# Kernel optimization log

Measured on AMD Instinct MI355X. Metric: run time of the kernel, lower is better.

## Reference

```python
import jax, jax.numpy as jnp
import numpy as np

B, F, T, H, LBL, NT = 64, 128, 1024, 256, 4, 11
S = T * LBL  # CRF sequence length


def setup_inputs() -> dict:
    key = jax.random.key(0)
    ks = iter(jax.random.split(key, 40))
    rn = lambda shape, s=1.0: jax.random.normal(next(ks), shape, jnp.float32) * s
    x = rn((B, F, T))
    lengths = jax.random.randint(next(ks), (B,), 1, T + 1)
    lengths = lengths.at[0].set(T)  # max(batch_length) == T
    labels = jax.random.randint(next(ks), (B, S), 0, NT)
    valid = jnp.arange(S)[None, :] < (lengths * LBL)[:, None]
    y_true = jnp.where(valid, labels, -1)
    sc = 0.05
    return dict(
        x=x, y_true=y_true, lengths=lengths,
        h0=rn((4, B, H)), c0=rn((4, B, H)),
        w_ih_l0=rn((4 * H, F), sc), w_hh_l0=rn((4 * H, H), sc), b_l0=rn((4 * H,), sc),
        w_ih_l0r=rn((4 * H, F), sc), w_hh_l0r=rn((4 * H, H), sc), b_l0r=rn((4 * H,), sc),
        w_ih_l1=rn((4 * H, 2 * H), sc), w_hh_l1=rn((4 * H, H), sc), b_l1=rn((4 * H,), sc),
        w_ih_l1r=rn((4 * H, 2 * H), sc), w_hh_l1r=rn((4 * H, H), sc), b_l1r=rn((4 * H,), sc),
        w_out=rn((LBL * NT, 2 * H), sc), b_out=rn((LBL * NT,), sc),
        start_trans=rn((NT,), 0.1), end_trans=rn((NT,), 0.1), trans=rn((NT, NT), 0.1),
    )


def _lstm_dir(x, h0, c0, w_ih, w_hh, b):
    # x: [B,T,Din] -> hs: [B,T,H]; PyTorch gate order i,f,g,o
    xg = jnp.einsum('btd,gd->btg', x, w_ih) + b  # [B,T,4H]

    def step(carry, xt):
        h, c = carry
        g = xt + h @ w_hh.T
        i, f, gg, o = jnp.split(g, 4, axis=-1)
        c = jax.nn.sigmoid(f) * c + jax.nn.sigmoid(i) * jnp.tanh(gg)
        h = jax.nn.sigmoid(o) * jnp.tanh(c)
        return (h, c), h

    _, hs = jax.lax.scan(step, (h0, c0), jnp.swapaxes(xg, 0, 1))
    return jnp.swapaxes(hs, 0, 1)


def _bilayer(x, rev_idx, h0f, c0f, h0b, c0b, pf, pb):
    hf = _lstm_dir(x, h0f, c0f, *pf)
    xr = jnp.take_along_axis(x, rev_idx[:, :, None], axis=1)  # per-sample reverse within length
    hbr = _lstm_dir(xr, h0b, c0b, *pb)
    hb = jnp.take_along_axis(hbr, rev_idx[:, :, None], axis=1)
    return jnp.concatenate([hf, hb], axis=-1)


def _crf_llh(em, tags, mask, start, end, trans):
    # em [B,S,NT], tags [B,S] (-1 pad), mask [B,S] bool. torchcrf sum-reduction llh.
    tc = jnp.where(mask, tags, 0)
    bidx = jnp.arange(em.shape[0])
    first = start[tc[:, 0]] + em[bidx, 0, tc[:, 0]]
    em_sc = jnp.take_along_axis(em, tc[:, :, None], axis=2)[..., 0]  # [B,S]
    tr_sc = trans[tc[:, :-1], tc[:, 1:]]  # [B,S-1]
    num = first + jnp.sum((tr_sc + em_sc[:, 1:]) * mask[:, 1:], axis=1)
    seq_ends = jnp.sum(mask, axis=1) - 1
    num = num + end[tc[bidx, seq_ends]]

    def step(alpha, inp):
        e, m = inp  # e [B,NT], m [B]
        nxt = jax.nn.logsumexp(alpha[:, :, None] + trans[None] + e[:, None, :], axis=1)
        return jnp.where(m[:, None], nxt, alpha), None

    alpha0 = start[None] + em[:, 0]
    alpha, _ = jax.lax.scan(step, alpha0, (jnp.swapaxes(em[:, 1:], 0, 1), mask[:, 1:].T))
    logZ = jax.nn.logsumexp(alpha + end[None], axis=1)
    return jnp.sum(num - logZ)


def _viterbi(em, mask, start, end, trans):
    def step(score, inp):
        e, m = inp
        nxt = score[:, :, None] + trans[None] + e[:, None, :]  # [B,NT,NT]
        best, idx = jnp.max(nxt, axis=1), jnp.argmax(nxt, axis=1)
        return jnp.where(m[:, None], best, score), idx

    score0 = start[None] + em[:, 0]
    final, hist = jax.lax.scan(step, score0, (jnp.swapaxes(em[:, 1:], 0, 1), mask[:, 1:].T))
    last = jnp.argmax(final + end[None], axis=1)  # [B]

    def back(carry, inp):
        h, m = inp  # h [B,NT], m [B]
        prev = jnp.take_along_axis(h, carry[:, None], axis=1)[:, 0]
        carry = jnp.where(m, prev, carry)
        return carry, carry

    _, ys = jax.lax.scan(back, last, (hist, mask[:, 1:].T), reverse=True)  # [S-1,B]
    return jnp.concatenate([ys.T, last[:, None]], axis=1)  # [B,S]


def reference(x, y_true, lengths, h0, c0,
              w_ih_l0, w_hh_l0, b_l0, w_ih_l0r, w_hh_l0r, b_l0r,
              w_ih_l1, w_hh_l1, b_l1, w_ih_l1r, w_hh_l1r, b_l1r,
              w_out, b_out, start_trans, end_trans, trans):
    xt = jnp.transpose(x, (0, 2, 1))  # [B,T,F]
    t = jnp.arange(T)
    rev_idx = jnp.where(t[None, :] < lengths[:, None], lengths[:, None] - 1 - t[None, :], t[None, :])
    l0 = _bilayer(xt, rev_idx, h0[0], c0[0], h0[1], c0[1],
                  (w_ih_l0, w_hh_l0, b_l0), (w_ih_l0r, w_hh_l0r, b_l0r))
    l1 = _bilayer(l0, rev_idx, h0[2], c0[2], h0[3], c0[3],
                  (w_ih_l1, w_hh_l1, b_l1), (w_ih_l1r, w_hh_l1r, b_l1r))
    feats = l1 * (t[None, :] < lengths[:, None])[:, :, None].astype(l1.dtype)  # pad -> 0 like pad_packed_sequence
    em = (feats @ w_out.T + b_out).reshape(B, S, NT)
    mask = y_true != -1
    loss = -_crf_llh(em, y_true, mask, start_trans, end_trans, trans) / B
    decoded = _viterbi(em, mask, start_trans, end_trans, trans)
    return loss, decoded
```

## Files before the change

### kernel.cpp

```cpp
#include <hip/hip_runtime.h>
#include <hip/hip_bf16.h>

typedef _Float16 f16x8 __attribute__((ext_vector_type(8)));
typedef float f32x4 __attribute__((ext_vector_type(4)));

#define DI static __device__ __forceinline__

constexpr int Bn = 64, Fn = 128, Tn = 1024, Hn = 256, NTn = 11;
constexpr int BT = Bn * Tn;
constexpr int Gn = 4 * Hn;
constexpr int Sn = 4 * Tn;

__device__ __align__(16) _Float16 g_xt_h[BT * Fn];
__device__ __align__(16) _Float16 g_xt_l[BT * Fn];
__device__ __align__(16) _Float16 g_f0_h[BT * 512];
__device__ __align__(16) _Float16 g_f0_l[BT * 512];
__device__ __align__(16) _Float16 g_f1_h[BT * 512];
__device__ __align__(16) _Float16 g_f1_l[BT * 512];
__device__ __align__(16) float    g_xg[(size_t)BT * 2048];
__device__ __align__(16) _Float16 g_whh_h[4 * Gn * Hn];
__device__ __align__(16) _Float16 g_whh_l[4 * Gn * Hn];
__device__ __align__(16) _Float16 g_wih0_h[2048 * Fn];
__device__ __align__(16) _Float16 g_wih0_l[2048 * Fn];
__device__ __align__(16) _Float16 g_wih1_h[2048 * 512];
__device__ __align__(16) _Float16 g_wih1_l[2048 * 512];
__device__ __align__(16) _Float16 g_wout_h[48 * 512];
__device__ __align__(16) _Float16 g_wout_l[48 * 512];
__device__ float g_b0[2048], g_b1[2048], g_bo[48];
__device__ float g_em[BT * 44];
__device__ __align__(4) unsigned char g_hist[(size_t)Sn * Bn * NTn];
__device__ int   g_rev[BT];
__device__ float g_llh[Bn];
__device__ int   g_last[Bn];
__device__ unsigned int g_hxs[2][4][2][4096];
__device__ int g_syncp[2][4][2][8][2][16];

DI f32x4 mfma_(f16x8 a, f16x8 b, f32x4 c) {
  return __builtin_amdgcn_mfma_f32_16x16x32_f16(a, b, c, 0, 0, 0);
}
DI float sigf(float x) { return 1.f / (1.f + __expf(-x)); }
DI float tanh_(float x) { return 1.f - 2.f / (1.f + __expf(2.f * x)); }

__global__ void k_zinit() {
  int i = blockIdx.x * 256 + threadIdx.x;
  if (i < 2 * 4 * 2 * 8 * 2 * 16) ((int*)g_syncp)[i] = 0;
}

__global__ void k_split(const float* __restrict__ src, int which, int off, int n) {
  int i = blockIdx.x * 256 + threadIdx.x;
  if (i >= n) return;
  float v = src[i];
  _Float16 h = (_Float16)v;
  _Float16 l = (_Float16)(v - (float)h);
  _Float16 *H, *L;
  switch (which) {
    case 1:  H = g_wih0_h; L = g_wih0_l; break;
    case 2:  H = g_wih1_h; L = g_wih1_l; break;
    default: H = g_wout_h; L = g_wout_l; break;
  }
  H[off + i] = h; L[off + i] = l;
}

__global__ void k_wswz(const float* __restrict__ w0, const float* __restrict__ w1,
                       const float* __restrict__ w2, const float* __restrict__ w3) {
  int i = blockIdx.x * 256 + threadIdx.x;
  if (i >= 4 * Gn * Hn) return;
  int mat = i >> 18;
  int e = i & 262143;
  int nt = e >> 12, rem = e & 4095;
  int kc = rem >> 9;
  int rem2 = rem & 511;
  int lane = rem2 >> 3, j = rem2 & 7;
  int row = nt * 16 + (lane & 15);
  int col = kc * 32 + (lane >> 4) * 8 + j;
  const float* src = mat == 0 ? w0 : mat == 1 ? w1 : mat == 2 ? w2 : w3;
  float v = src[row * Hn + col];
  _Float16 h = (_Float16)v;
  g_whh_h[i] = h;
  g_whh_l[i] = (_Float16)(v - (float)h);
}

__global__ void k_copy(const float* __restrict__ src, int which, int off, int n) {
  int i = blockIdx.x * 256 + threadIdx.x;
  if (i >= n) return;
  float* D = which == 0 ? g_b0 : which == 1 ? g_b1 : g_bo;
  D[off + i] = src[i];
}

__global__ void k_pad() {
  int i = blockIdx.x * 256 + threadIdx.x;
  if (i < 48 * 512 - 44 * 512) {
    g_wout_h[44 * 512 + i] = (_Float16)0.f;
    g_wout_l[44 * 512 + i] = (_Float16)0.f;
  }
  if (i < 4) g_bo[44 + i] = 0.f;
}

__global__ void k_rev(const int* __restrict__ lengths) {
  int i = blockIdx.x * 256 + threadIdx.x;
  if (i >= BT) return;
  int b = i >> 10, t = i & 1023;
  int len = lengths[b];
  int r = (t < len) ? (len - 1 - t) : t;
  g_rev[i] = (b << 10) | r;
}

__global__ void k_xpose(const float* __restrict__ x) {
  __shared__ float tile[32][33];
  int t0 = blockIdx.x * 32, d0 = blockIdx.y * 32, b = blockIdx.z;
  int tx = threadIdx.x, ty = threadIdx.y;
  #pragma unroll
  for (int i = 0; i < 4; i++) {
    int d = d0 + ty + i * 8;
    tile[ty + i * 8][tx] = x[((size_t)b * Fn + d) * Tn + t0 + tx];
  }
  __syncthreads();
  #pragma unroll
  for (int i = 0; i < 4; i++) {
    int t = t0 + ty + i * 8;
    float v = tile[tx][ty + i * 8];
    _Float16 h = (_Float16)v;
    size_t o = ((size_t)b * Tn + t) * Fn + d0 + tx;
    g_xt_h[o] = h;
    g_xt_l[o] = (_Float16)(v - (float)h);
  }
}

template <int SEL, int NPL>
__global__ __launch_bounds__(256) void k_gemm() {
  constexpr int KD = SEL == 0 ? 128 : 512;
  constexpr int WM = SEL == 2 ? 4 : 2;
  constexpr int WN = SEL == 2 ? 1 : 2;
  constexpr int MW = SEL == 2 ? 2 : 4;
  constexpr int NW = SEL == 2 ? 3 : 4;
  constexpr int LDO = SEL == 2 ? 44 : 2048;
  constexpr int NCOL = SEL == 2 ? 44 : 2048;
  constexpr int NSPLIT = SEL == 2 ? (1 << 30) : 1024;
  const _Float16* Ah = SEL == 0 ? g_xt_h : SEL == 1 ? g_f0_h : g_f1_h;
  const _Float16* Al = SEL == 0 ? g_xt_l : SEL == 1 ? g_f0_l : g_f1_l;
  const _Float16* Bh = SEL == 0 ? g_wih0_h : SEL == 1 ? g_wih1_h : g_wout_h;
  const _Float16* Bl = SEL == 0 ? g_wih0_l : SEL == 1 ? g_wih1_l : g_wout_l;
  const float* bias = SEL == 0 ? g_b0 : SEL == 1 ? g_b1 : g_bo;
  float* out = SEL == 2 ? g_em : g_xg;

  const int lane = threadIdx.x & 63, wv = threadIdx.x >> 6;
  const int wm = wv / WN, wn = wv % WN;
  const int c = lane & 15, q = lane >> 4;
  const int bm0 = blockIdx.x * (WM * MW * 16);
  const int bn0 = blockIdx.y * (WN * NW * 16);
  const bool bw = bn0 >= NSPLIT;
  int arow[MW];
  #pragma unroll
  for (int mi = 0; mi < MW; mi++) {
    int r = bm0 + (wm * MW + mi) * 16 + c;
    arow[mi] = bw ? g_rev[r] : r;
  }
  f32x4 acc[MW][NW];
  #pragma unroll
  for (int mi = 0; mi < MW; mi++)
    #pragma unroll
    for (int ni = 0; ni < NW; ni++) acc[mi][ni] = f32x4{0.f, 0.f, 0.f, 0.f};

  for (int kc = 0; kc < KD / 32; kc++) {
    const int k = kc * 32 + q * 8;
    f16x8 ah[MW], al[MW], bh[NW], bl[NW];
    #pragma unroll
    for (int mi = 0; mi < MW; mi++) {
      ah[mi] = *(const f16x8*)(Ah + (size_t)arow[mi] * KD + k);
      if constexpr (NPL > 1) al[mi] = *(const f16x8*)(Al + (size_t)arow[mi] * KD + k);
    }
    #pragma unroll
    for (int ni = 0; ni < NW; ni++) {
      int n = bn0 + (wn * NW + ni) * 16 + c;
      bh[ni] = *(const f16x8*)(Bh + (size_t)n * KD + k);
      if constexpr (NPL > 1) bl[ni] = *(const f16x8*)(Bl + (size_t)n * KD + k);
    }
    #pragma unroll
    for (int mi = 0; mi < MW; mi++)
      #pragma unroll
      for (int ni = 0; ni < NW; ni++) {
        acc[mi][ni] = mfma_(ah[mi], bh[ni], acc[mi][ni]);
        if constexpr (NPL > 1) {
          acc[mi][ni] = mfma_(ah[mi], bl[ni], acc[mi][ni]);
          acc[mi][ni] = mfma_(al[mi], bh[ni], acc[mi][ni]);
        }
      }
  }
  #pragma unroll
  for (int mi = 0; mi < MW; mi++)
    #pragma unroll
    for (int ni = 0; ni < NW; ni++) {
      int col = bn0 + (wn * NW + ni) * 16 + c;
      if (col < NCOL) {
        int row0 = bm0 + (wm * MW + mi) * 16 + q * 4;
        float bv = bias[col];
        #pragma unroll
        for (int r = 0; r < 4; r++)
          out[(size_t)(row0 + r) * LDO + col] = acc[mi][ni][r] + bv;
      }
    }
}

__global__ __launch_bounds__(512, 1) void k_rec3(const float* __restrict__ h0,
                                                 const float* __restrict__ c0, int layer) {
  __shared__ __align__(16) _Float16 Wh_l[8][8][512];
  __shared__ __align__(16) _Float16 Wl_l[8][8][512];
  __shared__ __align__(16) _Float16 lh[4096], ll[4096];
  __shared__ float gbuf[2][3][16][16];
  const int tid = threadIdx.x, lane = tid & 63, w = tid >> 6;
  const int c = lane & 15, q = lane >> 4;
  const int bg = blockIdx.x, d = blockIdx.y, s = blockIdx.z;
  const int dirIdx = layer * 2 + d;
  const int g = w >> 1, hm = w & 1;
  const int m = 2 * s + hm;
  const int nt = g * 16 + m;
  const int u = m * 16 + c;
  const _Float16* whp = g_whh_h + (size_t)dirIdx * (Gn * Hn);
  const _Float16* wlp = g_whh_l + (size_t)dirIdx * (Gn * Hn);
  _Float16* fh = layer ? g_f1_h : g_f0_h;
  _Float16* fl = layer ? g_f1_l : g_f0_l;
  const float* h0p = h0 + ((size_t)dirIdx * Bn + bg * 16) * Hn;
  const float* c0p = c0 + ((size_t)dirIdx * Bn + bg * 16) * Hn;

  #pragma unroll
  for (int kc = 0; kc < 8; kc++) {
    *(f16x8*)&Wh_l[w][kc][lane * 8] =
        *(const f16x8*)(whp + ((size_t)(nt * 8 + kc) * 64 + lane) * 8);
    *(f16x8*)&Wl_l[w][kc][lane * 8] =
        *(const f16x8*)(wlp + ((size_t)(nt * 8 + kc) * 64 + lane) * 8);
  }
  for (int i = tid; i < 4096; i += 512) {
    int j = i & 7, ln = (i >> 3) & 63, kc = i >> 9;
    int row = ln & 15, uu = kc * 32 + ((ln >> 4) * 8) + j;
    float v = h0p[row * Hn + uu];
    _Float16 hv = (_Float16)v;
    lh[i] = hv;
    ll[i] = (_Float16)(v - (float)hv);
  }
  float creg[4];
  if (g == 0) {
    #pragma unroll
    for (int r = 0; r < 4; r++) creg[r] = c0p[(4 * q + r) * Hn + u];
  }
  size_t xoff[4];
  #pragma unroll
  for (int r = 0; r < 4; r++)
    xoff[r] = ((size_t)(bg * 16 + 4 * q + r) * Tn) * 2048 + (size_t)d * 1024;
  const int col = g * 256 + u;
  const int fb = (((u >> 5) * 64 + ((u >> 3) & 3) * 16) * 8) + (u & 7);

  float xgv[4];
  #pragma unroll
  for (int r = 0; r < 4; r++) xgv[r] = g_xg[xoff[r] + col];
  __syncthreads();

  for (int t = 0; t < Tn; t++) {
    f32x4 acc;
    #pragma unroll
    for (int r = 0; r < 4; r++) acc[r] = xgv[r];

    #pragma unroll
    for (int kc = 0; kc < 8; kc++) {
      f16x8 ah = *(const f16x8*)(lh + (kc * 64 + lane) * 8);
      f16x8 al = *(const f16x8*)(ll + (kc * 64 + lane) * 8);
      f16x8 wh = *(const f16x8*)&Wh_l[w][kc][lane * 8];
      f16x8 wl = *(const f16x8*)&Wl_l[w][kc][lane * 8];
      acc = mfma_(ah, wh, acc);
      acc = mfma_(ah, wl, acc);
      acc = mfma_(al, wh, acc);
    }

    if (g != 0) {
      #pragma unroll
      for (int r = 0; r < 4; r++) gbuf[hm][g - 1][4 * q + r][c] = acc[r];
    }
    __syncthreads();

    const bool more = (t + 1 < Tn);
    if (g == 0) {
      _Float16 hvs[4], lvs[4];
      #pragma unroll
      for (int r = 0; r < 4; r++) {
        float gi = acc[r];
        float gf = gbuf[hm][0][4 * q + r][c];
        float gg = gbuf[hm][1][4 * q + r][c];
        float go = gbuf[hm][2][4 * q + r][c];
        float cn = sigf(gf) * creg[r] + sigf(gi) * tanh_(gg);
        float hn = sigf(go) * tanh_(cn);
        creg[r] = cn;
        hvs[r] = (_Float16)hn;
        lvs[r] = (_Float16)(hn - (float)hvs[r]);
        if (more) {
          unsigned int pk = (unsigned int)__builtin_bit_cast(unsigned short, hvs[r]) |
                            ((unsigned int)__builtin_bit_cast(unsigned short, lvs[r]) << 16);
          __hip_atomic_store(&g_hxs[t & 1][bg][d][fb + (4 * q + r) * 8], pk,
                             __ATOMIC_RELAXED, __HIP_MEMORY_SCOPE_AGENT);
        }
      }
      if (more) {
        asm volatile("s_waitcnt vmcnt(0)" ::: "memory");
        if (lane == 0)
          __hip_atomic_store(&g_syncp[layer][bg][d][s][hm][0], t + 1,
                             __ATOMIC_RELAXED, __HIP_MEMORY_SCOPE_AGENT);
      }
      #pragma unroll
      for (int r = 0; r < 4; r++) {
        int bi = bg * 16 + 4 * q + r;
        int rv = (d == 0) ? bi * Tn + t : g_rev[bi * Tn + t];
        size_t fo = (size_t)rv * 512 + d * 256 + u;
        fh[fo] = hvs[r];
        fl[fo] = lvs[r];
      }
    }

    if (more) {
      float xn[4];
      #pragma unroll
      for (int r = 0; r < 4; r++)
        xn[r] = g_xg[xoff[r] + (size_t)(t + 1) * 2048 + col];

      if (w == 7 && lane < 16) {
        const int* fp = &g_syncp[layer][bg][d][lane >> 1][lane & 1][0];
        while (__hip_atomic_load(fp, __ATOMIC_RELAXED, __HIP_MEMORY_SCOPE_AGENT) < t + 1)
          __builtin_amdgcn_s_sleep(1);
      }
      __syncthreads();

      const unsigned long long* s64 =
          (const unsigned long long*)&g_hxs[t & 1][bg][d][0];
      unsigned long long p0 = __hip_atomic_load(s64 + tid * 4 + 0, __ATOMIC_RELAXED,
                                                __HIP_MEMORY_SCOPE_AGENT);
      unsigned long long p1 = __hip_atomic_load(s64 + tid * 4 + 1, __ATOMIC_RELAXED,
                                                __HIP_MEMORY_SCOPE_AGENT);
      unsigned long long p2 = __hip_atomic_load(s64 + tid * 4 + 2, __ATOMIC_RELAXED,
                                                __HIP_MEMORY_SCOPE_AGENT);
      unsigned long long p3 = __hip_atomic_load(s64 + tid * 4 + 3, __ATOMIC_RELAXED,
                                                __HIP_MEMORY_SCOPE_AGENT);
      unsigned int w0 = (unsigned int)p0, w1 = (unsigned int)(p0 >> 32);
      unsigned int w2 = (unsigned int)p1, w3 = (unsigned int)(p1 >> 32);
      unsigned int w4 = (unsigned int)p2, w5 = (unsigned int)(p2 >> 32);
      unsigned int w6 = (unsigned int)p3, w7 = (unsigned int)(p3 >> 32);
      uint4 hiw, low;
      hiw.x = (w0 & 0xffffu) | (w1 << 16);
      hiw.y = (w2 & 0xffffu) | (w3 << 16);
      hiw.z = (w4 & 0xffffu) | (w5 << 16);
      hiw.w = (w6 & 0xffffu) | (w7 << 16);
      low.x = (w0 >> 16) | (w1 & 0xffff0000u);
      low.y = (w2 >> 16) | (w3 & 0xffff0000u);
      low.z = (w4 >> 16) | (w5 & 0xffff0000u);
      low.w = (w6 >> 16) | (w7 & 0xffff0000u);
      *(uint4*)&lh[tid * 8] = hiw;
      *(uint4*)&ll[tid * 8] = low;

      __syncthreads();
      #pragma unroll
      for (int r = 0; r < 4; r++) xgv[r] = xn[r];
    }
  }
}

__global__ __launch_bounds__(64) void k_scan(const int* __restrict__ lengths,
                                             const int* __restrict__ y_true,
                                             const float* __restrict__ start,
                                             const float* __restrict__ endt,
                                             const float* __restrict__ trans) {
  const int b = blockIdx.x, j = threadIdx.x;
  const int V = lengths[b] * 4;
  const float* em = g_em + (size_t)b * (Tn * 44);
  float tcol[11];
  #pragma unroll
  for (int i = 0; i < 11; i++) tcol[i] = (j < 11) ? trans[i * 11 + j] : 0.f;
  float alpha = (j < 11) ? start[j] + em[j] : -1e30f;
  float score = alpha;
  for (int s = 1; s < V; s++) {
    float e = (j < 11) ? em[s * 11 + j] : 0.f;
    float av[11];
    float m = -1e30f, bestv = -1e30f;
    int bi = 0;
    #pragma unroll
    for (int i = 0; i < 11; i++) {
      float ai = __shfl(alpha, i);
      float si = __shfl(score, i);
      float va = ai + tcol[i];
      float vs = si + tcol[i];
      av[i] = va;
      m = fmaxf(m, va);
      if (vs > bestv) { bestv = vs; bi = i; }
    }
    float sum = 0.f;
    #pragma unroll
    for (int i = 0; i < 11; i++) sum += __expf(av[i] - m);
    alpha = e + m + __logf(sum);
    score = bestv + e;
    if (j < 11) g_hist[(size_t)s * (Bn * NTn) + b * NTn + j] = (unsigned char)bi;
  }
  float ae = (j < 11) ? alpha + endt[j] : -1e30f;
  float se = (j < 11) ? score + endt[j] : -1e30f;
  float m2 = -1e30f;
  #pragma unroll
  for (int i = 0; i < 11; i++) m2 = fmaxf(m2, __shfl(ae, i));
  float s2 = 0.f;
  #pragma unroll
  for (int i = 0; i < 11; i++) s2 += __expf(__shfl(ae, i) - m2);
  float logZ = m2 + __logf(s2);
  float bv = -1e30f;
  int bj = 0;
  #pragma unroll
  for (int i = 0; i < 11; i++) {
    float v = __shfl(se, i);
    if (v > bv) { bv = v; bj = i; }
  }
  const int* y = y_true + (size_t)b * Sn;
  float part = 0.f;
  for (int s = 1 + j; s < V; s += 64) {
    int yp = y[s - 1], yc = y[s];
    part += trans[yp * 11 + yc] + em[s * 11 + yc];
  }
  #pragma unroll
  for (int off = 32; off > 0; off >>= 1) part += __shfl_down(part, off);
  if (j == 0) {
    int y0 = y[0];
    float num = start[y0] + em[y0] + part + endt[y[V - 1]];
    g_llh[b] = num - logZ;
    g_last[b] = bj;
  }
}

__global__ void k_loss(float* out) {
  if (threadIdx.x == 0 && blockIdx.x == 0) {
    float s = 0.f;
    for (int b = 0; b < Bn; b++) s += g_llh[b];
    out[0] = -s / (float)Bn;
  }
}

__global__ __launch_bounds__(256) void k_back(const int* __restrict__ lengths,
                                              float* __restrict__ out) {
  __shared__ unsigned char hbuf[64 * Bn * NTn];
  const int tid = threadIdx.x;
  int carry = 0, V = 0;
  if (tid < 64) {
    carry = g_last[tid];
    V = lengths[tid] * 4;
    out[1 + (size_t)tid * Sn + (Sn - 1)] = (float)carry;
  }
  for (int s0 = Sn - 64; s0 >= 0; s0 -= 64) {
    __syncthreads();
    const unsigned int* src = (const unsigned int*)(g_hist + (size_t)s0 * (Bn * NTn));
    unsigned int* dst = (unsigned int*)hbuf;
    for (int i = tid; i < 64 * Bn * NTn / 4; i += 256) dst[i] = src[i];
    __syncthreads();
    if (tid < 64) {
      for (int s = s0 + 63; s >= s0 && s >= 1; s--) {
        int pr = hbuf[(s - s0) * (Bn * NTn) + tid * NTn + carry];
        if (s < V) carry = pr;
        out[1 + (size_t)tid * Sn + (s - 1)] = (float)carry;
      }
    }
  }
}

extern "C" void kernel_launch(void* const* d_in, const int* in_sizes, int n_in,
                              void* d_out, int out_size, void* d_ws, size_t ws_size,
                              hipStream_t stream) {
  (void)in_sizes; (void)n_in; (void)d_ws; (void)ws_size; (void)out_size;
  const float* x        = (const float*)d_in[0];
  const int*   y_true   = (const int*)d_in[1];
  const int*   lengths  = (const int*)d_in[2];
  const float* h0       = (const float*)d_in[3];
  const float* c0       = (const float*)d_in[4];
  const float* w_ih_l0  = (const float*)d_in[5];
  const float* w_hh_l0  = (const float*)d_in[6];
  const float* b_l0     = (const float*)d_in[7];
  const float* w_ih_l0r = (const float*)d_in[8];
  const float* w_hh_l0r = (const float*)d_in[9];
  const float* b_l0r    = (const float*)d_in[10];
  const float* w_ih_l1  = (const float*)d_in[11];
  const float* w_hh_l1  = (const float*)d_in[12];
  const float* b_l1     = (const float*)d_in[13];
  const float* w_ih_l1r = (const float*)d_in[14];
  const float* w_hh_l1r = (const float*)d_in[15];
  const float* b_l1r    = (const float*)d_in[16];
  const float* w_out    = (const float*)d_in[17];
  const float* b_out    = (const float*)d_in[18];
  const float* start_t  = (const float*)d_in[19];
  const float* end_t    = (const float*)d_in[20];
  const float* trans    = (const float*)d_in[21];
  float* out = (float*)d_out;

  auto gs = [](int n) { return dim3((n + 255) / 256); };
  dim3 b256(256);

  k_zinit<<<gs(2048), b256, 0, stream>>>();
  k_wswz<<<gs(4 * Gn * Hn), b256, 0, stream>>>(w_hh_l0, w_hh_l0r, w_hh_l1, w_hh_l1r);
  k_split<<<gs(131072), b256, 0, stream>>>(w_ih_l0, 1, 0, 131072);
  k_split<<<gs(131072), b256, 0, stream>>>(w_ih_l0r, 1, 131072, 131072);
  k_split<<<gs(524288), b256, 0, stream>>>(w_ih_l1, 2, 0, 524288);
  k_split<<<gs(524288), b256, 0, stream>>>(w_ih_l1r, 2, 524288, 524288);
  k_split<<<gs(22528), b256, 0, stream>>>(w_out, 3, 0, 22528);
  k_copy<<<gs(1024), b256, 0, stream>>>(b_l0, 0, 0, 1024);
  k_copy<<<gs(1024), b256, 0, stream>>>(b_l0r, 0, 1024, 1024);
  k_copy<<<gs(1024), b256, 0, stream>>>(b_l1, 1, 0, 1024);
  k_copy<<<gs(1024), b256, 0, stream>>>(b_l1r, 1, 1024, 1024);
  k_copy<<<gs(44), b256, 0, stream>>>(b_out, 2, 0, 44);
  k_pad<<<gs(2048), b256, 0, stream>>>();
  k_rev<<<gs(BT), b256, 0, stream>>>(lengths);
  k_xpose<<<dim3(Tn / 32, Fn / 32, Bn), dim3(32, 8), 0, stream>>>(x);

  k_gemm<0, 3><<<dim3(BT / 128, 16), b256, 0, stream>>>();
  k_rec3<<<dim3(4, 2, 8), dim3(512), 0, stream>>>(h0, c0, 0);
  k_gemm<1, 3><<<dim3(BT / 128, 16), b256, 0, stream>>>();
  k_rec3<<<dim3(4, 2, 8), dim3(512), 0, stream>>>(h0, c0, 1);
  k_gemm<2, 3><<<dim3(BT / 128, 1), b256, 0, stream>>>();
  k_scan<<<dim3(Bn), dim3(64), 0, stream>>>(lengths, y_true, start_t, end_t, trans);
  k_loss<<<dim3(1), dim3(64), 0, stream>>>(out);
  k_back<<<dim3(1), b256, 0, stream>>>(lengths, out);
}
```

Before: 12.15 ms.

## Replace flag-based cross-block sync with tagged per-element hidden-state exchange

The separate sync-flag array is removed. Each published hidden-state word now carries a 32-bit tag encoding the layer and step, so consumers spin directly on the data words until every tag matches instead of polling flags and then reloading. The producing block also writes its own slice into LDS locally and skips the global read for its own slice. This removes the vmcnt wait, the flag store, one barrier and a round-trip on the recurrent critical path, at the cost of doubling exchange-buffer traffic and spinning on many words per thread.

```diff
diff --git a/kernel.cpp b/kernel.cpp
--- a/kernel.cpp
+++ b/kernel.cpp
@@ -32,8 +32,7 @@
 __device__ int   g_rev[BT];
 __device__ float g_llh[Bn];
 __device__ int   g_last[Bn];
-__device__ unsigned int g_hxs[2][4][2][4096];
-__device__ int g_syncp[2][4][2][8][2][16];
+__device__ unsigned long long g_hxs2[2][4][2][4096];
 
 DI f32x4 mfma_(f16x8 a, f16x8 b, f32x4 c) {
   return __builtin_amdgcn_mfma_f32_16x16x32_f16(a, b, c, 0, 0, 0);
@@ -43,7 +42,7 @@
 
 __global__ void k_zinit() {
   int i = blockIdx.x * 256 + threadIdx.x;
-  if (i < 2 * 4 * 2 * 8 * 2 * 16) ((int*)g_syncp)[i] = 0;
+  if (i < 2 * 4 * 2 * 4096) ((unsigned long long*)g_hxs2)[i] = 0ULL;
 }
 
 __global__ void k_split(const float* __restrict__ src, int which, int off, int n) {
@@ -277,6 +276,7 @@
     __syncthreads();
 
     const bool more = (t + 1 < Tn);
+    const unsigned int wantag = (unsigned int)(layer * 2048 + t + 1);
     if (g == 0) {
       _Float16 hvs[4], lvs[4];
       #pragma unroll
@@ -293,15 +293,13 @@
         if (more) {
           unsigned int pk = (unsigned int)__builtin_bit_cast(unsigned short, hvs[r]) |
                             ((unsigned int)__builtin_bit_cast(unsigned short, lvs[r]) << 16);
-          __hip_atomic_store(&g_hxs[t & 1][bg][d][fb + (4 * q + r) * 8], pk,
+          unsigned long long pv = ((unsigned long long)wantag << 32) | (unsigned long long)pk;
+          int idx = fb + (4 * q + r) * 8;
+          __hip_atomic_store(&g_hxs2[t & 1][bg][d][idx], pv,
                              __ATOMIC_RELAXED, __HIP_MEMORY_SCOPE_AGENT);
+          lh[idx] = hvs[r];
+          ll[idx] = lvs[r];
         }
-      }
-      if (more) {
-        asm volatile("s_waitcnt vmcnt(0)" ::: "memory");
-        if (lane == 0)
-          __hip_atomic_store(&g_syncp[layer][bg][d][s][hm][0], t + 1,
-                             __ATOMIC_RELAXED, __HIP_MEMORY_SCOPE_AGENT);
       }
       #pragma unroll
       for (int r = 0; r < 4; r++) {
@@ -319,38 +317,48 @@
       for (int r = 0; r < 4; r++)
         xn[r] = g_xg[xoff[r] + (size_t)(t + 1) * 2048 + col];
 
-      if (w == 7 && lane < 16) {
-        const int* fp = &g_syncp[layer][bg][d][lane >> 1][lane & 1][0];
-        while (__hip_atomic_load(fp, __ATOMIC_RELAXED, __HIP_MEMORY_SCOPE_AGENT) < t + 1)
-          __builtin_amdgcn_s_sleep(1);
+      if (w != s) {
+        const unsigned long long* s64 = &g_hxs2[t & 1][bg][d][0];
+        #define LD_(i) __hip_atomic_load(s64 + tid * 8 + i, __ATOMIC_RELAXED, \
+                                         __HIP_MEMORY_SCOPE_AGENT)
+        unsigned long long v0 = LD_(0), v1 = LD_(1), v2 = LD_(2), v3 = LD_(3);
+        unsigned long long v4 = LD_(4), v5 = LD_(5), v6 = LD_(6), v7 = LD_(7);
+        while (true) {
+          bool st0 = (unsigned int)(v0 >> 32) != wantag;
+          bool st1 = (unsigned int)(v1 >> 32) != wantag;
+          bool st2 = (unsigned int)(v2 >> 32) != wantag;
+          bool st3 = (unsigned int)(v3 >> 32) != wantag;
+          bool st4 = (unsigned int)(v4 >> 32) != wantag;
+          bool st5 = (unsigned int)(v5 >> 32) != wantag;
+          bool st6 = (unsigned int)(v6 >> 32) != wantag;
+          bool st7 = (unsigned int)(v7 >> 32) != wantag;
+          if (!(st0 | st1 | st2 | st3 | st4 | st5 | st6 | st7)) break;
+          if (st0) v0 = LD_(0);
+          if (st1) v1 = LD_(1);
+          if (st2) v2 = LD_(2);
+          if (st3) v3 = LD_(3);
+          if (st4) v4 = LD_(4);
+          if (st5) v5 = LD_(5);
+          if (st6) v6 = LD_(6);
+          if (st7) v7 = LD_(7);
+        }
+        #undef LD_
+        unsigned int w0 = (unsigned int)v0, w1 = (unsigned int)v1;
+        unsigned int w2 = (unsigned int)v2, w3 = (unsigned int)v3;
+        unsigned int w4 = (unsigned int)v4, w5 = (unsigned int)v5;
+        unsigned int w6 = (unsigned int)v6, w7 = (unsigned int)v7;
+        uint4 hiw, low;
+        hiw.x = (w0 & 0xffffu) | (w1 << 16);
+        hiw.y = (w2 & 0xffffu) | (w3 << 16);
+        hiw.z = (w4 & 0xffffu) | (w5 << 16);
+        hiw.w = (w6 & 0xffffu) | (w7 << 16);
+        low.x = (w0 >> 16) | (w1 & 0xffff0000u);
+        low.y = (w2 >> 16) | (w3 & 0xffff0000u);
+        low.z = (w4 >> 16) | (w5 & 0xffff0000u);
+        low.w = (w6 >> 16) | (w7 & 0xffff0000u);
+        *(uint4*)&lh[tid * 8] = hiw;
+        *(uint4*)&ll[tid * 8] = low;
       }
-      __syncthreads();
-
-      const unsigned long long* s64 =
-          (const unsigned long long*)&g_hxs[t & 1][bg][d][0];
-      unsigned long long p0 = __hip_atomic_load(s64 + tid * 4 + 0, __ATOMIC_RELAXED,
-                                                __HIP_MEMORY_SCOPE_AGENT);
-      unsigned long long p1 = __hip_atomic_load(s64 + tid * 4 + 1, __ATOMIC_RELAXED,
-                                                __HIP_MEMORY_SCOPE_AGENT);
-      unsigned long long p2 = __hip_atomic_load(s64 + tid * 4 + 2, __ATOMIC_RELAXED,
-                                                __HIP_MEMORY_SCOPE_AGENT);
-      unsigned long long p3 = __hip_atomic_load(s64 + tid * 4 + 3, __ATOMIC_RELAXED,
-                                                __HIP_MEMORY_SCOPE_AGENT);
-      unsigned int w0 = (unsigned int)p0, w1 = (unsigned int)(p0 >> 32);
-      unsigned int w2 = (unsigned int)p1, w3 = (unsigned int)(p1 >> 32);
-      unsigned int w4 = (unsigned int)p2, w5 = (unsigned int)(p2 >> 32);
-      unsigned int w6 = (unsigned int)p3, w7 = (unsigned int)(p3 >> 32);
-      uint4 hiw, low;
-      hiw.x = (w0 & 0xffffu) | (w1 << 16);
-      hiw.y = (w2 & 0xffffu) | (w3 << 16);
-      hiw.z = (w4 & 0xffffu) | (w5 << 16);
-      hiw.w = (w6 & 0xffffu) | (w7 << 16);
-      low.x = (w0 >> 16) | (w1 & 0xffff0000u);
-      low.y = (w2 >> 16) | (w3 & 0xffff0000u);
-      low.z = (w4 >> 16) | (w5 & 0xffff0000u);
-      low.w = (w6 >> 16) | (w7 & 0xffff0000u);
-      *(uint4*)&lh[tid * 8] = hiw;
-      *(uint4*)&ll[tid * 8] = low;
 
       __syncthreads();
       #pragma unroll
@@ -491,7 +499,7 @@
   auto gs = [](int n) { return dim3((n + 255) / 256); };
   dim3 b256(256);
 
-  k_zinit<<<gs(2048), b256, 0, stream>>>();
+  k_zinit<<<gs(65536), b256, 0, stream>>>();
   k_wswz<<<gs(4 * Gn * Hn), b256, 0, stream>>>(w_hh_l0, w_hh_l0r, w_hh_l1, w_hh_l1r);
   k_split<<<gs(131072), b256, 0, stream>>>(w_ih_l0, 1, 0, 131072);
   k_split<<<gs(131072), b256, 0, stream>>>(w_ih_l0r, 1, 131072, 131072);
```

Result: slower. 19.52 ms (+60.6%).

## Prefetch emissions in CRF scan, double-buffer backtrace history, fold loss into back kernel

Applied to the files above, without the earlier changes.

The CRF forward scan now loads emissions in batches of eight steps ahead of the dependent recurrence, so global-load latency is hidden. The Viterbi backtrace kernel double-buffers its history chunks in shared memory, with threads 64 and up copying the next chunk while the first 64 threads walk the current one. The separate loss-reduction kernel is folded into the backtrace kernel, saving a launch. The k_zinit grid is also doubled, which may be a correctness tweak. Costs are more registers in the scan and twice the shared memory in the back kernel.

```diff
diff --git a/kernel.cpp b/kernel.cpp
--- a/kernel.cpp
+++ b/kernel.cpp
@@ -372,27 +372,39 @@
   for (int i = 0; i < 11; i++) tcol[i] = (j < 11) ? trans[i * 11 + j] : 0.f;
   float alpha = (j < 11) ? start[j] + em[j] : -1e30f;
   float score = alpha;
-  for (int s = 1; s < V; s++) {
-    float e = (j < 11) ? em[s * 11 + j] : 0.f;
-    float av[11];
-    float m = -1e30f, bestv = -1e30f;
-    int bi = 0;
-    #pragma unroll
-    for (int i = 0; i < 11; i++) {
-      float ai = __shfl(alpha, i);
-      float si = __shfl(score, i);
-      float va = ai + tcol[i];
-      float vs = si + tcol[i];
-      av[i] = va;
-      m = fmaxf(m, va);
-      if (vs > bestv) { bestv = vs; bi = i; }
-    }
-    float sum = 0.f;
-    #pragma unroll
-    for (int i = 0; i < 11; i++) sum += __expf(av[i] - m);
-    alpha = e + m + __logf(sum);
-    score = bestv + e;
-    if (j < 11) g_hist[(size_t)s * (Bn * NTn) + b * NTn + j] = (unsigned char)bi;
+  for (int s0 = 1; s0 < V; s0 += 8) {
+    float eb[8];
+    #pragma unroll
+    for (int k = 0; k < 8; k++) {
+      int s = s0 + k;
+      eb[k] = (j < 11 && s < Sn) ? em[s * 11 + j] : 0.f;
+    }
+    #pragma unroll
+    for (int k = 0; k < 8; k++) {
+      int s = s0 + k;
+      if (s < V) {
+        float e = eb[k];
+        float av[11];
+        float m = -1e30f, bestv = -1e30f;
+        int bi = 0;
+        #pragma unroll
+        for (int i = 0; i < 11; i++) {
+          float ai = __shfl(alpha, i);
+          float si = __shfl(score, i);
+          float va = ai + tcol[i];
+          float vs = si + tcol[i];
+          av[i] = va;
+          m = fmaxf(m, va);
+          if (vs > bestv) { bestv = vs; bi = i; }
+        }
+        float sum = 0.f;
+        #pragma unroll
+        for (int i = 0; i < 11; i++) sum += __expf(av[i] - m);
+        alpha = e + m + __logf(sum);
+        score = bestv + e;
+        if (j < 11) g_hist[(size_t)s * (Bn * NTn) + b * NTn + j] = (unsigned char)bi;
+      }
+    }
   }
   float ae = (j < 11) ? alpha + endt[j] : -1e30f;
   float se = (j < 11) ? score + endt[j] : -1e30f;
@@ -426,37 +438,47 @@
   }
 }
 
-__global__ void k_loss(float* out) {
-  if (threadIdx.x == 0 && blockIdx.x == 0) {
-    float s = 0.f;
-    for (int b = 0; b < Bn; b++) s += g_llh[b];
-    out[0] = -s / (float)Bn;
-  }
-}
-
 __global__ __launch_bounds__(256) void k_back(const int* __restrict__ lengths,
                                               float* __restrict__ out) {
-  __shared__ unsigned char hbuf[64 * Bn * NTn];
+  __shared__ unsigned char hbuf[2][64 * Bn * NTn];
   const int tid = threadIdx.x;
+  if (tid == 0) {
+    float ssum = 0.f;
+    for (int b = 0; b < Bn; b++) ssum += g_llh[b];
+    out[0] = -ssum / (float)Bn;
+  }
   int carry = 0, V = 0;
   if (tid < 64) {
     carry = g_last[tid];
     V = lengths[tid] * 4;
     out[1 + (size_t)tid * Sn + (Sn - 1)] = (float)carry;
   }
-  for (int s0 = Sn - 64; s0 >= 0; s0 -= 64) {
-    __syncthreads();
-    const unsigned int* src = (const unsigned int*)(g_hist + (size_t)s0 * (Bn * NTn));
-    unsigned int* dst = (unsigned int*)hbuf;
-    for (int i = tid; i < 64 * Bn * NTn / 4; i += 256) dst[i] = src[i];
-    __syncthreads();
+  constexpr int CHW = 64 * Bn * NTn / 4;
+  const int nc = Sn / 64;
+  {
+    const unsigned int* src =
+        (const unsigned int*)(g_hist + (size_t)(nc - 1) * 64 * (Bn * NTn));
+    unsigned int* dst = (unsigned int*)hbuf[(nc - 1) & 1];
+    for (int i = tid; i < CHW; i += 256) dst[i] = src[i];
+  }
+  __syncthreads();
+  for (int c = nc - 1; c >= 0; c--) {
+    if (c > 0 && tid >= 64) {
+      const unsigned int* src =
+          (const unsigned int*)(g_hist + (size_t)(c - 1) * 64 * (Bn * NTn));
+      unsigned int* dst = (unsigned int*)hbuf[(c - 1) & 1];
+      for (int i = tid - 64; i < CHW; i += 192) dst[i] = src[i];
+    }
     if (tid < 64) {
+      const unsigned char* hb = hbuf[c & 1];
+      const int s0 = c * 64;
       for (int s = s0 + 63; s >= s0 && s >= 1; s--) {
-        int pr = hbuf[(s - s0) * (Bn * NTn) + tid * NTn + carry];
+        int pr = hb[(s - s0) * (Bn * NTn) + tid * NTn + carry];
         if (s < V) carry = pr;
         out[1 + (size_t)tid * Sn + (s - 1)] = (float)carry;
       }
     }
+    __syncthreads();
   }
 }
 
@@ -491,7 +513,7 @@
   auto gs = [](int n) { return dim3((n + 255) / 256); };
   dim3 b256(256);
 
-  k_zinit<<<gs(2048), b256, 0, stream>>>();
+  k_zinit<<<gs(4096), b256, 0, stream>>>();
   k_wswz<<<gs(4 * Gn * Hn), b256, 0, stream>>>(w_hh_l0, w_hh_l0r, w_hh_l1, w_hh_l1r);
   k_split<<<gs(131072), b256, 0, stream>>>(w_ih_l0, 1, 0, 131072);
   k_split<<<gs(131072), b256, 0, stream>>>(w_ih_l0r, 1, 131072, 131072);
@@ -513,6 +535,5 @@
   k_rec3<<<dim3(4, 2, 8), dim3(512), 0, stream>>>(h0, c0, 1);
   k_gemm<2, 3><<<dim3(BT / 128, 1), b256, 0, stream>>>();
   k_scan<<<dim3(Bn), dim3(64), 0, stream>>>(lengths, y_true, start_t, end_t, trans);
-  k_loss<<<dim3(1), dim3(64), 0, stream>>>(out);
   k_back<<<dim3(1), b256, 0, stream>>>(lengths, out);
 }
```

Measured after the change: 11.85 ms. 2.5% less time.
